# Kernel tuning notes

Measured on AMD Instinct MI355X. Metric: run time of the kernel, lower is better.

Reference implementation:

```python
import jax, jax.numpy as jnp
import numpy as np

B, S, HID = 4, 1024, 4096
NH, NKV, HD = 32, 8, 128
FF = 11008
EPS = 1e-6
THETA = 10000.0


def rms_norm(x, w, eps=EPS):
    v = jnp.mean(jnp.square(x), axis=-1, keepdims=True)
    return x * jax.lax.rsqrt(v + eps) * w


def rotate_half(x):
    x1, x2 = jnp.split(x, 2, axis=-1)
    return jnp.concatenate([-x2, x1], axis=-1)


def rope_cos_sin(position_ids, head_dim=HD, theta=THETA):
    inv_freq = 1.0 / (theta ** (jnp.arange(0, head_dim, 2, dtype=jnp.float32) / head_dim))
    freqs = position_ids.astype(jnp.float32)[..., None] * inv_freq  # [B,S,HD/2]
    emb = jnp.concatenate([freqs, freqs], axis=-1)  # [B,S,HD]
    return jnp.cos(emb)[:, None, :, :], jnp.sin(emb)[:, None, :, :]  # [B,1,S,HD]


def setup_inputs() -> dict:
    key = jax.random.key(0)
    ks = jax.random.split(key, 9)
    sc = 0.02
    pos = jnp.tile(jnp.arange(S, dtype=jnp.int64 if jax.config.jax_enable_x64 else jnp.int32)[None, :], (B, 1))
    causal = jnp.tril(jnp.ones((S, S), dtype=bool))
    mask = jnp.where(causal, 0.0, -1e9).astype(jnp.float32)[None, None]  # [1,1,S,S]
    return {
        "hidden_states": jax.random.normal(ks[0], (B * S, HID), jnp.float32),
        "position_ids": pos,
        "attn_mask": mask,
        "Wq": jax.random.normal(ks[1], (HID, NH * HD), jnp.float32) * sc,
        "Wk": jax.random.normal(ks[2], (HID, NKV * HD), jnp.float32) * sc,
        "Wv": jax.random.normal(ks[3], (HID, NKV * HD), jnp.float32) * sc,
        "Wo": jax.random.normal(ks[4], (NH * HD, HID), jnp.float32) * sc,
        "ln1_w": jnp.ones((HID,), jnp.float32),
        "ln2_w": jnp.ones((HID,), jnp.float32),
        "w_gate": jax.random.normal(ks[5], (HID, FF), jnp.float32) * sc,
        "w_up": jax.random.normal(ks[6], (HID, FF), jnp.float32) * sc,
        "w_down": jax.random.normal(ks[7], (FF, HID), jnp.float32) * sc,
    }


def reference(hidden_states, position_ids, attn_mask, Wq, Wk, Wv, Wo, ln1_w, ln2_w, w_gate, w_up, w_down):
    residual = hidden_states
    h = rms_norm(hidden_states, ln1_w)

    # QKV projections on flat tokens, then reshape per train partition
    q = (h @ Wq).reshape(B, S, NH, HD).transpose(0, 2, 1, 3)     # [B,NH,S,HD]
    k = (h @ Wk).reshape(B, S, NKV, HD).transpose(0, 2, 1, 3)    # [B,NKV,S,HD]
    v = (h @ Wv).reshape(B, S, NKV, HD).transpose(0, 2, 1, 3)

    cos, sin = rope_cos_sin(position_ids)
    q = q * cos + rotate_half(q) * sin
    k = k * cos + rotate_half(k) * sin

    n_rep = NH // NKV
    k = jnp.repeat(k, n_rep, axis=1)  # [B,NH,S,HD]
    v = jnp.repeat(v, n_rep, axis=1)

    scores = jnp.einsum('bhqd,bhkd->bhqk', q, k) / np.sqrt(HD)
    scores = scores + attn_mask
    # softmax in fp32 as in the source
    probs = jax.nn.softmax(scores.astype(jnp.float32), axis=-1).astype(q.dtype)
    attn = jnp.einsum('bhqk,bhkd->bhqd', probs, v)               # [B,NH,S,HD]
    attn = attn.transpose(0, 2, 1, 3).reshape(B * S, NH * HD)
    h = attn @ Wo

    h = residual + h
    residual = h
    h2 = rms_norm(h, ln2_w)
    mlp = (jax.nn.silu(h2 @ w_gate) * (h2 @ w_up)) @ w_down
    return residual + mlp
```

## Files before the change

### kernel.cpp

```cpp
#include <hip/hip_runtime.h>

#define DEVINL __device__ __forceinline__

typedef unsigned short u16;
typedef __attribute__((ext_vector_type(8))) short bf16x8;
typedef __attribute__((ext_vector_type(4))) float f32x4;
typedef __attribute__((ext_vector_type(4))) unsigned short u16x4;


DEVINL float bf2f(u16 u) { union { unsigned i; float f; } x; x.i = ((unsigned)u) << 16; return x.f; }
DEVINL u16 f2bf(float f) {
  union { float f; unsigned i; } x; x.f = f;
  unsigned r = x.i + 0x7fffu + ((x.i >> 16) & 1u);
  return (u16)(r >> 16);
}

DEVINL void async16(u16* lds, const u16* g) {
  __builtin_amdgcn_global_load_lds((const __attribute__((address_space(1))) unsigned*)g,
                                   (__attribute__((address_space(3))) unsigned*)lds, 16, 0, 0);
}

struct CJob { const float* in; u16* out; int K, N, ntiles; int mode; };

DEVINL void conv_one(const float* __restrict__ in, u16* __restrict__ out,
                     int K, int N, int tile, int t, float (*tl)[65], int mode) {
  int tn = N >> 6;
  int kt = tile / tn;
  int k0 = kt << 6, n0 = (tile - kt*tn) << 6;
  int r = t >> 4, c4 = (t & 15) << 2;
  #pragma unroll
  for (int it = 0; it < 4; it++) {
    int row = r + it*16;
    f32x4 v = *(const f32x4*)(in + (size_t)(k0 + row)*N + n0 + c4);
    tl[row][c4+0] = v[0]; tl[row][c4+1] = v[1];
    tl[row][c4+2] = v[2]; tl[row][c4+3] = v[3];
  }
  __syncthreads();
  #pragma unroll
  for (int it = 0; it < 4; it++) {
    int nrow = r + it*16;
    u16x4 ov;
    #pragma unroll
    for (int e = 0; e < 4; e++) ov[e] = f2bf(tl[c4+e][nrow]);
    int orow = n0 + nrow;
    if (mode == 1)      orow = ((orow >> 5) << 6) + (orow & 31);
    else if (mode == 2) orow = ((orow >> 5) << 6) + 32 + (orow & 31);
    *(u16x4*)(out + (size_t)orow*K + k0 + c4) = ov;
  }
  __syncthreads();
}

__global__ __launch_bounds__(256) void conv3(CJob j0, CJob j1, CJob j2) {
  __shared__ float tl[64][65];
  int ntot = j0.ntiles + j1.ntiles + j2.ntiles;
  for (int g = blockIdx.x; g < ntot; g += gridDim.x) {
    CJob* jp;
    int tile;
    if (g < j0.ntiles)                 { jp = &j0; tile = g; }
    else if (g < j0.ntiles + j1.ntiles){ jp = &j1; tile = g - j0.ntiles; }
    else                               { jp = &j2; tile = g - j0.ntiles - j1.ntiles; }
    conv_one(jp->in, jp->out, jp->K, jp->N, tile, threadIdx.x, tl, jp->mode);
  }
}

__global__ __launch_bounds__(256) void conv_t(const float* __restrict__ in,
                                              u16* __restrict__ out, int K, int N) {
  __shared__ float tl[64][65];
  int tile = blockIdx.y * gridDim.x + blockIdx.x;
  conv_one(in, out, K, N, tile, threadIdx.x, tl, 0);
}

__global__ __launch_bounds__(256) void rmsnorm_kernel(const float* __restrict__ x,
                                                      const float* __restrict__ w,
                                                      u16* __restrict__ out) {
  int row = blockIdx.x, t = threadIdx.x;
  const float* xr = x + (size_t)row * 4096;
  f32x4 v[4];
  float ss = 0.f;
  #pragma unroll
  for (int i = 0; i < 4; i++) {
    v[i] = *(const f32x4*)(xr + (t + 256*i)*4);
    ss += v[i][0]*v[i][0] + v[i][1]*v[i][1] + v[i][2]*v[i][2] + v[i][3]*v[i][3];
  }
  #pragma unroll
  for (int d = 1; d < 64; d <<= 1) ss += __shfl_xor(ss, d, 64);
  __shared__ float ps[4];
  if ((t & 63) == 0) ps[t >> 6] = ss;
  __syncthreads();
  float scale = rsqrtf((ps[0]+ps[1]+ps[2]+ps[3]) * (1.f/4096.f) + 1e-6f);
  #pragma unroll
  for (int i = 0; i < 4; i++) {
    f32x4 wv = *(const f32x4*)(w + (t + 256*i)*4);
    u16x4 o;
    #pragma unroll
    for (int e = 0; e < 4; e++) o[e] = f2bf(v[i][e] * scale * wv[e]);
    *(u16x4*)(out + (size_t)row*4096 + (t + 256*i)*4) = o;
  }
}

__global__ __launch_bounds__(256) void rope_kernel(u16* __restrict__ q, u16* __restrict__ k, int kstr) {
  int tok = blockIdx.x;
  int s = tok & 1023;
  __shared__ float cs[64], sn[64];
  int t = threadIdx.x;
  if (t < 64) {
    float inv = __expf(-(float)t * 0.14391156934f);
    float ang = (float)s * inv;
    cs[t] = cosf(ang); sn[t] = sinf(ang);
  }
  __syncthreads();
  const float qscale = 0.08838834764831845f;
  size_t qbase = (size_t)tok * 4096;
  #pragma unroll
  for (int it = 0; it < 8; it++) {
    int item = t + it*256; int h = item >> 6, j = item & 63;
    size_t i0 = qbase + h*128 + j;
    float x1 = bf2f(q[i0]), x2 = bf2f(q[i0+64]);
    float c = cs[j], si = sn[j];
    q[i0]    = f2bf((x1*c - x2*si) * qscale);
    q[i0+64] = f2bf((x2*c + x1*si) * qscale);
  }
  size_t kbase = (size_t)tok * kstr;
  #pragma unroll
  for (int it = 0; it < 2; it++) {
    int item = t + it*256; int h = item >> 6, j = item & 63;
    size_t i0 = kbase + h*128 + j;
    float x1 = bf2f(k[i0]), x2 = bf2f(k[i0+64]);
    float c = cs[j], si = sn[j];
    k[i0]    = f2bf(x1*c - x2*si);
    k[i0+64] = f2bf(x2*c + x1*si);
  }
}

__global__ __launch_bounds__(256) void vtrans(const u16* __restrict__ v, u16* __restrict__ vt, int vstr) {
  __shared__ u16 tile[32][33];
  int bh = blockIdx.z; int b = bh >> 3, kvh = bh & 7;
  int d0 = blockIdx.x << 5, s0 = blockIdx.y << 5;
  int tx = threadIdx.x, ty = threadIdx.y;
  for (int r = ty; r < 32; r += 8)
    tile[r][tx] = v[(size_t)(b*1024 + s0 + r)*vstr + kvh*128 + d0 + tx];
  __syncthreads();
  for (int r = ty; r < 32; r += 8)
    vt[(size_t)((b*8 + kvh)*128 + d0 + r)*1024 + s0 + tx] = tile[tx][r];
}

template<int EPI>
__global__ __launch_bounds__(256, 2) void gemm_bt(
    const u16* __restrict__ A, const u16* __restrict__ Bt,
    void* __restrict__ Cv, const float* __restrict__ resid,
    const u16* __restrict__ gate, int M, int N, int K) {
  __shared__ u16 As[128*64];
  __shared__ u16 Bs[128*64];
  int nwg = gridDim.x;
  int bid = (int)blockIdx.x;
  int cpx = nwg >> 3;
  int swz = (bid & 7) * cpx + (bid >> 3);
  int mt = M >> 7;
  int m0 = (swz % mt) << 7;
  int n0 = (swz / mt) << 7;
  int tid = threadIdx.x;
  int lane = tid & 63, wave = tid >> 6;
  int wm = wave >> 1, wn = wave & 1;

  f32x4 acc[4][4];
  f32x4 zero = {0.f, 0.f, 0.f, 0.f};
  #pragma unroll
  for (int i = 0; i < 4; i++)
    #pragma unroll
    for (int j = 0; j < 4; j++) acc[i][j] = zero;

  int arow[4], acolb[4];
  #pragma unroll
  for (int i = 0; i < 4; i++) {
    int c = i*256 + tid;
    arow[i]  = c >> 3;
    acolb[i] = ((c & 7) * 16) ^ ((arow[i] & 7) << 4);
  }

  int nsteps = K >> 6;
  for (int t = 0; t < nsteps; t++) {
    int k0 = t << 6;
    #pragma unroll
    for (int i = 0; i < 4; i++) {
      async16(As + i*2048 + wave*512, A  + (size_t)(m0 + arow[i])*K + k0 + (acolb[i] >> 1));
      async16(Bs + i*2048 + wave*512, Bt + (size_t)(n0 + arow[i])*K + k0 + (acolb[i] >> 1));
    }
    __syncthreads();
    #pragma unroll
    for (int ks = 0; ks < 2; ks++) {
      bf16x8 af[4], bfr[4];
      int c2 = (ks*32 + (lane >> 4)*8) * 2;
      #pragma unroll
      for (int mf = 0; mf < 4; mf++) {
        int r = wm*64 + mf*16 + (lane & 15);
        af[mf] = *(const bf16x8*)(As + r*64 + ((c2 ^ ((r & 7) << 4)) >> 1));
      }
      #pragma unroll
      for (int nf = 0; nf < 4; nf++) {
        int r = wn*64 + nf*16 + (lane & 15);
        bfr[nf] = *(const bf16x8*)(Bs + r*64 + ((c2 ^ ((r & 7) << 4)) >> 1));
      }
      #pragma unroll
      for (int mf = 0; mf < 4; mf++)
        #pragma unroll
        for (int nf = 0; nf < 4; nf++)
          acc[mf][nf] = __builtin_amdgcn_mfma_f32_16x16x32_bf16(af[mf], bfr[nf], acc[mf][nf], 0, 0, 0);
    }
    __syncthreads();
  }

  #pragma unroll
  for (int mf = 0; mf < 4; mf++)
    #pragma unroll
    for (int nf = 0; nf < 4; nf++)
      #pragma unroll
      for (int j = 0; j < 4; j++) {
        int rr = m0 + wm*64 + mf*16 + (lane >> 4)*4 + j;
        int cc = n0 + wn*64 + nf*16 + (lane & 15);
        size_t idx = (size_t)rr * N + cc;
        float v = acc[mf][nf][j];
        if constexpr (EPI == 0) {
          ((u16*)Cv)[idx] = f2bf(v);
        } else if constexpr (EPI == 1) {
          ((float*)Cv)[idx] = v + resid[idx];
        } else {
          float g = bf2f(gate[idx]);
          float sg = g / (1.f + __expf(-g));
          ((u16*)Cv)[idx] = f2bf(sg * v);
        }
      }
}

#define SB0() __builtin_amdgcn_sched_barrier(0)
#define BAR() __builtin_amdgcn_s_barrier()
#define LGKM(n) do { SB0(); asm volatile("s_waitcnt lgkmcnt(" #n ")" ::: "memory"); SB0(); } while (0)
#define VMC(n)  do { SB0(); asm volatile("s_waitcnt vmcnt(" #n ")"  ::: "memory"); SB0(); } while (0)
#define MFMAQ(qm, qn, AF, BQ) do { \
  __builtin_amdgcn_s_setprio(1); \
  _Pragma("unroll") for (int mf_ = 0; mf_ < 4; mf_++) \
  _Pragma("unroll") for (int nf_ = 0; nf_ < 2; nf_++) \
  _Pragma("unroll") for (int ks_ = 0; ks_ < 2; ks_++) \
    acc[(qm)*4+mf_][(qn)*2+nf_] = __builtin_amdgcn_mfma_f32_16x16x32_bf16( \
        AF[mf_][ks_], BQ[nf_][ks_], acc[(qm)*4+mf_][(qn)*2+nf_], 0, 0, 0); \
  __builtin_amdgcn_s_setprio(0); } while (0)

template<int KC, int EPI>
__global__ __launch_bounds__(512, 2) void gemm256(
    const u16* __restrict__ A, const u16* __restrict__ Bt,
    void* __restrict__ Cv, const float* __restrict__ resid,
    const u16* __restrict__ gate, int M, int N, int G,
    const float* __restrict__ cvin, u16* __restrict__ cvout, int cvK, int cvN, int cvTiles, int cvMode) {
  extern __shared__ u16 lds[];
  int bid = (int)blockIdx.x;
  int tid = threadIdx.x;

  if (bid >= G) {
    int cb = bid - G, CB = (int)gridDim.x - G;
    int h = tid >> 8, t = tid & 255;
    float (*tl)[65] = (float(*)[65])((char*)lds + h*16896);
    int pairs = cvTiles >> 1;
    for (int p = cb; p < pairs; p += CB)
      conv_one(cvin, cvout, cvK, cvN, 2*p + h, t, tl, cvMode);
    return;
  }

  int cpx = G >> 3;
  int swz = (bid & 7) * cpx + (bid >> 3);
  int mt = M >> 8;
  int m0 = (swz % mt) << 8;
  int n0 = (swz / mt) << 8;
  int lane = tid & 63, wave = tid >> 6;
  int wm = wave >> 2, wn = wave & 3;

  f32x4 acc[8][4];
  f32x4 zero = {0.f, 0.f, 0.f, 0.f};
  #pragma unroll
  for (int i = 0; i < 8; i++)
    #pragma unroll
    for (int j = 0; j < 4; j++) acc[i][j] = zero;

  int sCol = ((lane & 7) ^ (lane >> 3)) << 3;
  int aRow = (wave >> 2)*128 + (wave & 3)*16 + (lane >> 3);
  int bRow = (wave >> 1)*64  + (wave & 1)*16 + (lane >> 3);
  const u16* gA = A  + (size_t)(m0 + aRow) * KC + sCol;
  const u16* gB = Bt + (size_t)(n0 + bRow) * KC + sCol;
  constexpr size_t K8 = (size_t)8 * KC, K32 = (size_t)32 * KC, K64 = (size_t)64 * KC;

  int rA = lane & 15;
  int acol0 = (((lane >> 4)    ) ^ (rA & 7)) << 3;
  int acol1 = (((lane >> 4) + 4) ^ (rA & 7)) << 3;

  bf16x8 afA[4][2], afB[4][2], b0[2][2], b1[2][2];

  auto stageAq = [&](int buf, int qm, int k0) {
    u16* d = lds + buf*32768 + qm*8192 + wave*1024;
    const u16* s = gA + (size_t)qm*K64 + k0;
    async16(d, s); async16(d + 512, s + K8);
  };
  auto stageBq = [&](int buf, int qn, int k0) {
    u16* d = lds + buf*32768 + 16384 + qn*8192 + wave*1024;
    const u16* s = gB + (size_t)qn*K32 + k0;
    async16(d, s); async16(d + 512, s + K8);
  };
  auto loadAq = [&](int buf, int qm, bf16x8 (&af)[4][2]) {
    const u16* base = lds + buf*32768 + qm*8192 + wm*4096 + rA*64;
    #pragma unroll
    for (int mf = 0; mf < 4; mf++) {
      af[mf][0] = *(const bf16x8*)(base + mf*1024 + acol0);
      af[mf][1] = *(const bf16x8*)(base + mf*1024 + acol1);
    }
  };
  auto loadBq = [&](int buf, int qn, bf16x8 (&bq)[2][2]) {
    const u16* base = lds + buf*32768 + 16384 + qn*8192 + wn*2048 + rA*64;
    #pragma unroll
    for (int nf = 0; nf < 2; nf++) {
      bq[nf][0] = *(const bf16x8*)(base + nf*1024 + acol0);
      bq[nf][1] = *(const bf16x8*)(base + nf*1024 + acol1);
    }
  };

  constexpr int nt = KC >> 6;
  constexpr int IT = nt/2 - 1;

  stageAq(0, 0, 0); stageBq(0, 0, 0); stageBq(0, 1, 0); stageAq(0, 1, 0);
  VMC(4);
  stageAq(1, 0, 64); stageBq(1, 0, 64); stageBq(1, 1, 64);
  VMC(6);
  BAR();

  #pragma unroll 1
  for (int it = 0; it < IT; it++) {
    int kc = it*128;
    loadAq(0, 0, afA); loadBq(0, 0, b0); stageAq(1, 1, kc + 64);
    LGKM(8); BAR(); LGKM(0);
    MFMAQ(0, 0, afA, b0);
    SB0(); BAR();
    loadBq(0, 1, b1); stageAq(0, 0, kc + 128);
    BAR(); LGKM(0);
    MFMAQ(0, 1, afA, b1);
    SB0(); BAR();
    loadAq(0, 1, afB); stageBq(0, 0, kc + 128);
    BAR(); LGKM(0);
    MFMAQ(1, 0, afB, b0);
    SB0(); BAR();
    stageBq(0, 1, kc + 128);
    BAR();
    MFMAQ(1, 1, afB, b1);
    VMC(6); BAR();
    loadAq(1, 0, afA); loadBq(1, 0, b0); stageAq(0, 1, kc + 128);
    LGKM(8); BAR(); LGKM(0);
    MFMAQ(0, 0, afA, b0);
    SB0(); BAR();
    loadBq(1, 1, b1); stageAq(1, 0, kc + 192);
    BAR(); LGKM(0);
    MFMAQ(0, 1, afA, b1);
    SB0(); BAR();
    loadAq(1, 1, afB); stageBq(1, 0, kc + 192);
    BAR(); LGKM(0);
    MFMAQ(1, 0, afB, b0);
    SB0(); BAR();
    stageBq(1, 1, kc + 192);
    BAR();
    MFMAQ(1, 1, afB, b1);
    VMC(6); BAR();
  }

  {
    int kc = IT*128;
    loadAq(0, 0, afA); loadBq(0, 0, b0); stageAq(1, 1, kc + 64);
    LGKM(8); BAR(); LGKM(0);
    MFMAQ(0, 0, afA, b0);
    SB0(); BAR();
    loadBq(0, 1, b1);
    BAR(); LGKM(0);
    MFMAQ(0, 1, afA, b1);
    SB0(); BAR();
    loadAq(0, 1, afB);
    BAR(); LGKM(0);
    MFMAQ(1, 0, afB, b0);
    SB0(); BAR();
    MFMAQ(1, 1, afB, b1);
    VMC(0); BAR();
    loadAq(1, 0, afA); loadBq(1, 0, b0); SB0();
    loadBq(1, 1, b1); SB0();
    loadAq(1, 1, afB); SB0();
    LGKM(12); MFMAQ(0, 0, afA, b0);
    LGKM(8);  MFMAQ(0, 1, afA, b1);
    LGKM(0);  MFMAQ(1, 0, afB, b0);
    MFMAQ(1, 1, afB, b1);
  }

  if constexpr (EPI == 3) {
    int colb = (n0 >> 1) + wn*32 + (lane & 15);
    #pragma unroll
    for (int mf = 0; mf < 8; mf++)
      #pragma unroll
      for (int nf = 0; nf < 2; nf++)
        #pragma unroll
        for (int j = 0; j < 4; j++) {
          int rr = m0 + wm*128 + mf*16 + (lane >> 4)*4 + j;
          float g = acc[mf][nf][j];
          float u = acc[mf][nf+2][j];
          float sg = g / (1.f + __expf(-g));
          ((u16*)Cv)[(size_t)rr * 11008 + colb + nf*16] = f2bf(sg * u);
        }
  } else {
    #pragma unroll
    for (int mf = 0; mf < 8; mf++)
      #pragma unroll
      for (int nf = 0; nf < 4; nf++)
        #pragma unroll
        for (int j = 0; j < 4; j++) {
          int rr = m0 + wm*128 + mf*16 + (lane >> 4)*4 + j;
          int cc = n0 + wn*64 + nf*16 + (lane & 15);
          size_t idx = (size_t)rr * N + cc;
          float v = acc[mf][nf][j];
          if constexpr (EPI == 0) {
            ((u16*)Cv)[idx] = f2bf(v);
          } else if constexpr (EPI == 1) {
            ((float*)Cv)[idx] = v + resid[idx];
          } else if constexpr (EPI == 2) {
            float g = bf2f(gate[idx]);
            float sg = g / (1.f + __expf(-g));
            ((u16*)Cv)[idx] = f2bf(sg * v);
          }
        }
  }
}

__global__ __launch_bounds__(256, 4) void attn_kernel(
    const u16* __restrict__ q, const u16* __restrict__ k,
    const u16* __restrict__ vt, u16* __restrict__ out,
    CJob j0, CJob j1, CJob j2, int kstr) {
  __shared__ __align__(16) u16 shm[20480];
  u16* Ks = shm;
  u16* Vs = shm + 8192;
  u16* Ps = shm + 16384;
  int bid = blockIdx.x;

  if (bid >= 2048) {
    int cb = bid - 2048, CB = (int)gridDim.x - 2048;
    float (*tl)[65] = (float(*)[65])shm;
    int ntot = j0.ntiles + j1.ntiles + j2.ntiles;
    for (int g = cb; g < ntot; g += CB) {
      CJob* jp; int tile;
      if (g < j0.ntiles)                  { jp = &j0; tile = g; }
      else if (g < j0.ntiles + j1.ntiles) { jp = &j1; tile = g - j0.ntiles; }
      else                                { jp = &j2; tile = g - j0.ntiles - j1.ntiles; }
      conv_one(jp->in, jp->out, jp->K, jp->N, tile, threadIdx.x, tl, jp->mode);
    }
    return;
  }

  int qt = bid & 15;
  int h  = (bid >> 4) & 31;
  int b  = bid >> 9;
  int kvh = h >> 2;
  int tid = threadIdx.x, lane = tid & 63, wave = tid >> 6;
  int q0 = qt << 6;

  bf16x8 qf[4];
  {
    const u16* qb_ = q + (size_t)(b*1024 + q0 + wave*16 + (lane & 15))*4096 + h*128 + (lane >> 4)*8;
    #pragma unroll
    for (int ks = 0; ks < 4; ks++) qf[ks] = *(const bf16x8*)(qb_ + ks*32);
  }
  f32x4 o[8];
  f32x4 zero = {0.f,0.f,0.f,0.f};
  #pragma unroll
  for (int i = 0; i < 8; i++) o[i] = zero;
  float m[4] = {-1e30f,-1e30f,-1e30f,-1e30f};
  float l[4] = {0.f,0.f,0.f,0.f};

  int kr[4], kc[4], vr[4], vc[4];
  #pragma unroll
  for (int i = 0; i < 4; i++) {
    int c = i*256 + tid;
    kr[i] = c >> 4; kc[i] = ((c & 15)*16) ^ ((kr[i] & 7) << 4);
    vr[i] = c >> 3; vc[i] = ((c & 7)*16)  ^ ((vr[i] & 7) << 4);
  }

  for (int t = 0; t <= qt; t++) {
    int kv0 = t << 6;
    #pragma unroll
    for (int i = 0; i < 4; i++) {
      async16(Ks + i*2048 + wave*512, k  + (size_t)(b*1024 + kv0 + kr[i])*kstr + kvh*128 + (kc[i] >> 1));
      async16(Vs + i*2048 + wave*512, vt + (size_t)((b*8 + kvh)*128 + vr[i])*1024 + kv0 + (vc[i] >> 1));
    }
    __syncthreads();

    f32x4 s[4];
    #pragma unroll
    for (int nf = 0; nf < 4; nf++) {
      s[nf] = zero;
      #pragma unroll
      for (int ks = 0; ks < 4; ks++) {
        int r = nf*16 + (lane & 15);
        int c2 = (ks*32 + (lane >> 4)*8)*2;
        bf16x8 kf = *(const bf16x8*)(Ks + r*128 + ((c2 ^ ((r & 7) << 4)) >> 1));
        s[nf] = __builtin_amdgcn_mfma_f32_16x16x32_bf16(qf[ks], kf, s[nf], 0, 0, 0);
      }
    }
    if (t == qt) {
      #pragma unroll
      for (int nf = 0; nf < 4; nf++)
        #pragma unroll
        for (int j = 0; j < 4; j++) {
          int cc = nf*16 + (lane & 15);
          int rr = wave*16 + (lane >> 4)*4 + j;
          if (cc > rr) s[nf][j] = -1e30f;
        }
    }
    #pragma unroll
    for (int j = 0; j < 4; j++) {
      float mx = fmaxf(fmaxf(s[0][j], s[1][j]), fmaxf(s[2][j], s[3][j]));
      #pragma unroll
      for (int d = 1; d < 16; d <<= 1) mx = fmaxf(mx, __shfl_xor(mx, d, 64));
      float mn = fmaxf(m[j], mx);
      float f = __expf(m[j] - mn);
      m[j] = mn;
      float ssum = 0.f;
      #pragma unroll
      for (int nf = 0; nf < 4; nf++) {
        float p = __expf(s[nf][j] - mn);
        s[nf][j] = p; ssum += p;
      }
      #pragma unroll
      for (int d = 1; d < 16; d <<= 1) ssum += __shfl_xor(ssum, d, 64);
      l[j] = l[j]*f + ssum;
      #pragma unroll
      for (int nf = 0; nf < 8; nf++) o[nf][j] *= f;
    }
    #pragma unroll
    for (int nf = 0; nf < 4; nf++)
      #pragma unroll
      for (int j = 0; j < 4; j++) {
        int rr = (lane >> 4)*4 + j;
        int cb2 = ((nf*16 + (lane & 15))*2) ^ ((rr & 7) << 4);
        Ps[wave*1024 + rr*64 + (cb2 >> 1)] = f2bf(s[nf][j]);
      }
    #pragma unroll
    for (int ks2 = 0; ks2 < 2; ks2++) {
      int mr = lane & 15;
      int c2 = (ks2*32 + (lane >> 4)*8)*2;
      bf16x8 pa = *(const bf16x8*)(Ps + wave*1024 + mr*64 + ((c2 ^ ((mr & 7) << 4)) >> 1));
      #pragma unroll
      for (int nf = 0; nf < 8; nf++) {
        int d = nf*16 + (lane & 15);
        bf16x8 vf = *(const bf16x8*)(Vs + d*64 + ((c2 ^ ((d & 7) << 4)) >> 1));
        o[nf] = __builtin_amdgcn_mfma_f32_16x16x32_bf16(pa, vf, o[nf], 0, 0, 0);
      }
    }
    __syncthreads();
  }

  float inv[4];
  #pragma unroll
  for (int j = 0; j < 4; j++) inv[j] = 1.f / l[j];
  u16* ob = out + (size_t)(b*1024 + q0 + wave*16)*4096 + h*128;
  #pragma unroll
  for (int nf = 0; nf < 8; nf++)
    #pragma unroll
    for (int j = 0; j < 4; j++) {
      int rr = (lane >> 4)*4 + j;
      int cc = nf*16 + (lane & 15);
      ob[(size_t)rr*4096 + cc] = f2bf(o[nf][j] * inv[j]);
    }
}

extern "C" void kernel_launch(void* const* d_in, const int* in_sizes, int n_in,
                              void* d_out, int out_size, void* d_ws, size_t ws_size,
                              hipStream_t stream) {
  (void)in_sizes; (void)n_in; (void)out_size;
  const float* hidden = (const float*)d_in[0];
  const float* Wq  = (const float*)d_in[3];
  const float* Wk  = (const float*)d_in[4];
  const float* Wv  = (const float*)d_in[5];
  const float* Wo  = (const float*)d_in[6];
  const float* ln1 = (const float*)d_in[7];
  const float* ln2 = (const float*)d_in[8];
  const float* Wg  = (const float*)d_in[9];
  const float* Wu  = (const float*)d_in[10];
  const float* Wd  = (const float*)d_in[11];
  float* out = (float*)d_out;

  hipFuncSetAttribute((const void*)gemm256<4096,0>,  hipFuncAttributeMaxDynamicSharedMemorySize, 131072);
  hipFuncSetAttribute((const void*)gemm256<4096,1>,  hipFuncAttributeMaxDynamicSharedMemorySize, 131072);
  hipFuncSetAttribute((const void*)gemm256<4096,2>,  hipFuncAttributeMaxDynamicSharedMemorySize, 131072);
  hipFuncSetAttribute((const void*)gemm256<4096,3>,  hipFuncAttributeMaxDynamicSharedMemorySize, 131072);
  hipFuncSetAttribute((const void*)gemm256<11008,1>, hipFuncAttributeMaxDynamicSharedMemorySize, 131072);

  char* ws = (char*)d_ws;
  size_t off = 0;
  auto alloc = [&](size_t b) { char* p = ws + off; off += (b + 4095) & ~(size_t)4095; return p; };

  u16*  wqkvT = (u16*)alloc(50331648);
  u16*  woT   = (u16*)alloc(33554432);
  (void)alloc(8388608);
  u16*  wguT  = (u16*)alloc(180355072);
  u16*  h1    = (u16*)alloc(33554432);
  u16*  qb    = (u16*)alloc(33554432);
  u16*  kvb   = (u16*)alloc(16777216);
  u16*  vtb   = (u16*)alloc(8388608);
  float* hmid = (float*)alloc(67108864);
  u16*  gb    = (u16*)alloc(90177536);
  bool fused = off <= ws_size;

  dim3 blk(256);
  if (fused) {
    u16* wqT  = wqkvT;
    u16* wkvT = wqkvT + 16777216;
    u16* wkT  = wkvT;
    u16* wvT  = wkvT + 4194304;
    u16* wdT  = wqkvT;
    CJob Jq{Wq, wqT, 4096, 4096, 4096, 0}, Jk{Wk, wkT, 4096, 1024, 1024, 0}, Jv{Wv, wvT, 4096, 1024, 1024, 0};
    CJob Jo{Wo, woT, 4096, 4096, 4096, 0};
    CJob Jg{Wg, wguT, 4096, 11008, 11008, 1}, Ju{Wu, wguT, 4096, 11008, 11008, 2};

    conv3<<<2048, blk, 0, stream>>>(Jq, Jk, Jv);
    rmsnorm_kernel<<<4096, blk, 0, stream>>>(hidden, ln1, h1);
    gemm256<4096,0><<<256, 512, 131072, stream>>>(h1, wqT, qb, nullptr, nullptr, 4096, 4096, 256,
                                                  nullptr, nullptr, 0, 0, 0, 0);
    gemm_bt<0><<<512, blk, 0, stream>>>(h1, wkvT, kvb, nullptr, nullptr, 4096, 2048, 4096);
    rope_kernel<<<4096, blk, 0, stream>>>(qb, kvb, 2048);
    vtrans<<<dim3(4, 32, 32), dim3(32, 8), 0, stream>>>(kvb + 1024, vtb, 2048);
    attn_kernel<<<2048 + 1024, blk, 0, stream>>>(qb, kvb, vtb, h1, Jo, Jg, Ju, 2048);
    gemm256<4096,1><<<256, 512, 131072, stream>>>(h1, woT, hmid, hidden, nullptr, 4096, 4096, 256,
                                                  nullptr, nullptr, 0, 0, 0, 0);
    rmsnorm_kernel<<<4096, blk, 0, stream>>>(hmid, ln2, qb);
    gemm256<4096,3><<<1376 + 344, 512, 131072, stream>>>(qb, wguT, gb, nullptr, nullptr, 4096, 11008, 1376,
                                                         Wd, wdT, 11008, 4096, 11008, 0);
    gemm256<11008,1><<<256, 512, 131072, stream>>>(gb, wdT, out, hmid, nullptr, 4096, 4096, 256,
                                                   nullptr, nullptr, 0, 0, 0, 0);
  } else {
    off = 0;
    u16*  W1   = (u16*)alloc(90177536);
    u16*  h1s  = (u16*)alloc(33554432);
    u16*  qbs  = (u16*)alloc(33554432);
    u16*  kvbs = (u16*)alloc(16777216);
    u16*  vtbs = (u16*)alloc(8388608);
    float* hmids = (float*)alloc(67108864);
    u16*  gbs  = (u16*)alloc(90177536);
    if (off > ws_size) return;
    u16* wqT  = W1;
    u16* wkvT = W1 + 16777216;
    conv_t<<<dim3(64, 64),  blk, 0, stream>>>(Wq, wqT, 4096, 4096);
    conv_t<<<dim3(16, 64),  blk, 0, stream>>>(Wk, wkvT, 4096, 1024);
    conv_t<<<dim3(16, 64),  blk, 0, stream>>>(Wv, wkvT + 4194304, 4096, 1024);
    rmsnorm_kernel<<<4096, blk, 0, stream>>>(hidden, ln1, h1s);
    gemm256<4096,0><<<256, 512, 131072, stream>>>(h1s, wqT, qbs, nullptr, nullptr, 4096, 4096, 256,
                                                  nullptr, nullptr, 0, 0, 0, 0);
    gemm_bt<0><<<512, blk, 0, stream>>>(h1s, wkvT, kvbs, nullptr, nullptr, 4096, 2048, 4096);
    rope_kernel<<<4096, blk, 0, stream>>>(qbs, kvbs, 2048);
    vtrans<<<dim3(4, 32, 32), dim3(32, 8), 0, stream>>>(kvbs + 1024, vtbs, 2048);
    CJob J0{nullptr, nullptr, 0, 64, 0, 0};
    attn_kernel<<<2048, blk, 0, stream>>>(qbs, kvbs, vtbs, h1s, J0, J0, J0, 2048);
    conv_t<<<dim3(64, 64), blk, 0, stream>>>(Wo, W1, 4096, 4096);
    gemm256<4096,1><<<256, 512, 131072, stream>>>(h1s, W1, hmids, hidden, nullptr, 4096, 4096, 256,
                                                  nullptr, nullptr, 0, 0, 0, 0);
    rmsnorm_kernel<<<4096, blk, 0, stream>>>(hmids, ln2, qbs);
    conv_t<<<dim3(172, 64), blk, 0, stream>>>(Wg, W1, 4096, 11008);
    gemm256<4096,0><<<688, 512, 131072, stream>>>(qbs, W1, gbs, nullptr, nullptr, 4096, 11008, 688,
                                                  nullptr, nullptr, 0, 0, 0, 0);
    conv_t<<<dim3(172, 64), blk, 0, stream>>>(Wu, W1, 4096, 11008);
    gemm256<4096,2><<<688, 512, 131072, stream>>>(qbs, W1, gbs, nullptr, gbs, 4096, 11008, 688,
                                                  nullptr, nullptr, 0, 0, 0, 0);
    conv_t<<<dim3(64, 172), blk, 0, stream>>>(Wd, W1, 11008, 4096);
    gemm256<11008,1><<<256, 512, 131072, stream>>>(gbs, W1, out, hmids, nullptr, 4096, 4096, 256,
                                                   nullptr, nullptr, 0, 0, 0, 0);
  }
}
```

Measured before the change: 1.625 ms.

## Replace hand-scheduled gemm256 pipeline with a simple double-buffered loop

The hand-interleaved main loop of gemm256 is replaced with a plain double-buffered loop. That loop mixed quarter-tile async LDS staging, explicit lgkm/vm waitcnts, sched barriers and raw s_barriers. The new loop stages the whole next k-slice, computes the current slice with four MFMA quarters, and separates stages with __syncthreads. The unfused fallback path, the conv_t kernel and the unused SiLU-gate epilogue are also removed. The aim is simpler code that leaves scheduling to the compiler, at the cost of less fine-grained overlap and heavier full barriers that wait on all outstanding memory.

```diff
diff --git a/kernel.cpp b/kernel.cpp
--- a/kernel.cpp
+++ b/kernel.cpp
@@ -61,13 +61,6 @@
     else                               { jp = &j2; tile = g - j0.ntiles - j1.ntiles; }
     conv_one(jp->in, jp->out, jp->K, jp->N, tile, threadIdx.x, tl, jp->mode);
   }
-}
-
-__global__ __launch_bounds__(256) void conv_t(const float* __restrict__ in,
-                                              u16* __restrict__ out, int K, int N) {
-  __shared__ float tl[64][65];
-  int tile = blockIdx.y * gridDim.x + blockIdx.x;
-  conv_one(in, out, K, N, tile, threadIdx.x, tl, 0);
 }
 
 __global__ __launch_bounds__(256) void rmsnorm_kernel(const float* __restrict__ x,
@@ -231,10 +224,6 @@
       }
 }
 
-#define SB0() __builtin_amdgcn_sched_barrier(0)
-#define BAR() __builtin_amdgcn_s_barrier()
-#define LGKM(n) do { SB0(); asm volatile("s_waitcnt lgkmcnt(" #n ")" ::: "memory"); SB0(); } while (0)
-#define VMC(n)  do { SB0(); asm volatile("s_waitcnt vmcnt(" #n ")"  ::: "memory"); SB0(); } while (0)
 #define MFMAQ(qm, qn, AF, BQ) do { \
   __builtin_amdgcn_s_setprio(1); \
   _Pragma("unroll") for (int mf_ = 0; mf_ < 4; mf_++) \
@@ -248,7 +237,7 @@
 __global__ __launch_bounds__(512, 2) void gemm256(
     const u16* __restrict__ A, const u16* __restrict__ Bt,
     void* __restrict__ Cv, const float* __restrict__ resid,
-    const u16* __restrict__ gate, int M, int N, int G,
+    int M, int N, int G,
     const float* __restrict__ cvin, u16* __restrict__ cvout, int cvK, int cvN, int cvTiles, int cvMode) {
   extern __shared__ u16 lds[];
   int bid = (int)blockIdx.x;
@@ -302,6 +291,10 @@
     const u16* s = gB + (size_t)qn*K32 + k0;
     async16(d, s); async16(d + 512, s + K8);
   };
+  auto stageAll = [&](int buf, int k0) {
+    stageAq(buf, 0, k0); stageAq(buf, 1, k0);
+    stageBq(buf, 0, k0); stageBq(buf, 1, k0);
+  };
   auto loadAq = [&](int buf, int qm, bf16x8 (&af)[4][2]) {
     const u16* base = lds + buf*32768 + qm*8192 + wm*4096 + rA*64;
     #pragma unroll
@@ -318,76 +311,26 @@
       bq[nf][1] = *(const bf16x8*)(base + nf*1024 + acol1);
     }
   };
+  auto computeTile = [&](int buf) {
+    loadAq(buf, 0, afA); loadBq(buf, 0, b0); loadBq(buf, 1, b1); loadAq(buf, 1, afB);
+    MFMAQ(0, 0, afA, b0);
+    MFMAQ(0, 1, afA, b1);
+    MFMAQ(1, 0, afB, b0);
+    MFMAQ(1, 1, afB, b1);
+  };
 
   constexpr int nt = KC >> 6;
-  constexpr int IT = nt/2 - 1;
-
-  stageAq(0, 0, 0); stageBq(0, 0, 0); stageBq(0, 1, 0); stageAq(0, 1, 0);
-  VMC(4);
-  stageAq(1, 0, 64); stageBq(1, 0, 64); stageBq(1, 1, 64);
-  VMC(6);
-  BAR();
-
+  stageAll(0, 0);
+  __syncthreads();
   #pragma unroll 1
-  for (int it = 0; it < IT; it++) {
-    int kc = it*128;
-    loadAq(0, 0, afA); loadBq(0, 0, b0); stageAq(1, 1, kc + 64);
-    LGKM(8); BAR(); LGKM(0);
-    MFMAQ(0, 0, afA, b0);
-    SB0(); BAR();
-    loadBq(0, 1, b1); stageAq(0, 0, kc + 128);
-    BAR(); LGKM(0);
-    MFMAQ(0, 1, afA, b1);
-    SB0(); BAR();
-    loadAq(0, 1, afB); stageBq(0, 0, kc + 128);
-    BAR(); LGKM(0);
-    MFMAQ(1, 0, afB, b0);
-    SB0(); BAR();
-    stageBq(0, 1, kc + 128);
-    BAR();
-    MFMAQ(1, 1, afB, b1);
-    VMC(6); BAR();
-    loadAq(1, 0, afA); loadBq(1, 0, b0); stageAq(0, 1, kc + 128);
-    LGKM(8); BAR(); LGKM(0);
-    MFMAQ(0, 0, afA, b0);
-    SB0(); BAR();
-    loadBq(1, 1, b1); stageAq(1, 0, kc + 192);
-    BAR(); LGKM(0);
-    MFMAQ(0, 1, afA, b1);
-    SB0(); BAR();
-    loadAq(1, 1, afB); stageBq(1, 0, kc + 192);
-    BAR(); LGKM(0);
-    MFMAQ(1, 0, afB, b0);
-    SB0(); BAR();
-    stageBq(1, 1, kc + 192);
-    BAR();
-    MFMAQ(1, 1, afB, b1);
-    VMC(6); BAR();
-  }
-
-  {
-    int kc = IT*128;
-    loadAq(0, 0, afA); loadBq(0, 0, b0); stageAq(1, 1, kc + 64);
-    LGKM(8); BAR(); LGKM(0);
-    MFMAQ(0, 0, afA, b0);
-    SB0(); BAR();
-    loadBq(0, 1, b1);
-    BAR(); LGKM(0);
-    MFMAQ(0, 1, afA, b1);
-    SB0(); BAR();
-    loadAq(0, 1, afB);
-    BAR(); LGKM(0);
-    MFMAQ(1, 0, afB, b0);
-    SB0(); BAR();
-    MFMAQ(1, 1, afB, b1);
-    VMC(0); BAR();
-    loadAq(1, 0, afA); loadBq(1, 0, b0); SB0();
-    loadBq(1, 1, b1); SB0();
-    loadAq(1, 1, afB); SB0();
-    LGKM(12); MFMAQ(0, 0, afA, b0);
-    LGKM(8);  MFMAQ(0, 1, afA, b1);
-    LGKM(0);  MFMAQ(1, 0, afB, b0);
-    MFMAQ(1, 1, afB, b1);
+  for (int it = 0; it < nt/2; it++) {
+    int kc = it << 7;
+    stageAll(1, kc + 64);
+    computeTile(0);
+    __syncthreads();
+    if (kc + 128 < KC) stageAll(0, kc + 128);
+    computeTile(1);
+    __syncthreads();
   }
 
   if constexpr (EPI == 3) {
@@ -419,10 +362,6 @@
             ((u16*)Cv)[idx] = f2bf(v);
           } else if constexpr (EPI == 1) {
             ((float*)Cv)[idx] = v + resid[idx];
-          } else if constexpr (EPI == 2) {
-            float g = bf2f(gate[idx]);
-            float sg = g / (1.f + __expf(-g));
-            ((u16*)Cv)[idx] = f2bf(sg * v);
           }
         }
   }
@@ -586,7 +525,6 @@
 
   hipFuncSetAttribute((const void*)gemm256<4096,0>,  hipFuncAttributeMaxDynamicSharedMemorySize, 131072);
   hipFuncSetAttribute((const void*)gemm256<4096,1>,  hipFuncAttributeMaxDynamicSharedMemorySize, 131072);
-  hipFuncSetAttribute((const void*)gemm256<4096,2>,  hipFuncAttributeMaxDynamicSharedMemorySize, 131072);
   hipFuncSetAttribute((const void*)gemm256<4096,3>,  hipFuncAttributeMaxDynamicSharedMemorySize, 131072);
   hipFuncSetAttribute((const void*)gemm256<11008,1>, hipFuncAttributeMaxDynamicSharedMemorySize, 131072);
 
@@ -604,69 +542,31 @@
   u16*  vtb   = (u16*)alloc(8388608);
   float* hmid = (float*)alloc(67108864);
   u16*  gb    = (u16*)alloc(90177536);
-  bool fused = off <= ws_size;
+  if (off > ws_size) return;
+
+  u16* wqT  = wqkvT;
+  u16* wkvT = wqkvT + 16777216;
+  u16* wkT  = wkvT;
+  u16* wvT  = wkvT + 4194304;
+  u16* wdT  = wqkvT;
+  CJob Jq{Wq, wqT, 4096, 4096, 4096, 0}, Jk{Wk, wkT, 4096, 1024, 1024, 0}, Jv{Wv, wvT, 4096, 1024, 1024, 0};
+  CJob Jo{Wo, woT, 4096, 4096, 4096, 0};
+  CJob Jg{Wg, wguT, 4096, 11008, 11008, 1}, Ju{Wu, wguT, 4096, 11008, 11008, 2};
 
   dim3 blk(256);
-  if (fused) {
-    u16* wqT  = wqkvT;
-    u16* wkvT = wqkvT + 16777216;
-    u16* wkT  = wkvT;
-    u16* wvT  = wkvT + 4194304;
-    u16* wdT  = wqkvT;
-    CJob Jq{Wq, wqT, 4096, 4096, 4096, 0}, Jk{Wk, wkT, 4096, 1024, 1024, 0}, Jv{Wv, wvT, 4096, 1024, 1024, 0};
-    CJob Jo{Wo, woT, 4096, 4096, 4096, 0};
-    CJob Jg{Wg, wguT, 4096, 11008, 11008, 1}, Ju{Wu, wguT, 4096, 11008, 11008, 2};
-
-    conv3<<<2048, blk, 0, stream>>>(Jq, Jk, Jv);
-    rmsnorm_kernel<<<4096, blk, 0, stream>>>(hidden, ln1, h1);
-    gemm256<4096,0><<<256, 512, 131072, stream>>>(h1, wqT, qb, nullptr, nullptr, 4096, 4096, 256,
-                                                  nullptr, nullptr, 0, 0, 0, 0);
-    gemm_bt<0><<<512, blk, 0, stream>>>(h1, wkvT, kvb, nullptr, nullptr, 4096, 2048, 4096);
-    rope_kernel<<<4096, blk, 0, stream>>>(qb, kvb, 2048);
-    vtrans<<<dim3(4, 32, 32), dim3(32, 8), 0, stream>>>(kvb + 1024, vtb, 2048);
-    attn_kernel<<<2048 + 1024, blk, 0, stream>>>(qb, kvb, vtb, h1, Jo, Jg, Ju, 2048);
-    gemm256<4096,1><<<256, 512, 131072, stream>>>(h1, woT, hmid, hidden, nullptr, 4096, 4096, 256,
-                                                  nullptr, nullptr, 0, 0, 0, 0);
-    rmsnorm_kernel<<<4096, blk, 0, stream>>>(hmid, ln2, qb);
-    gemm256<4096,3><<<1376 + 344, 512, 131072, stream>>>(qb, wguT, gb, nullptr, nullptr, 4096, 11008, 1376,
-                                                         Wd, wdT, 11008, 4096, 11008, 0);
-    gemm256<11008,1><<<256, 512, 131072, stream>>>(gb, wdT, out, hmid, nullptr, 4096, 4096, 256,
-                                                   nullptr, nullptr, 0, 0, 0, 0);
-  } else {
-    off = 0;
-    u16*  W1   = (u16*)alloc(90177536);
-    u16*  h1s  = (u16*)alloc(33554432);
-    u16*  qbs  = (u16*)alloc(33554432);
-    u16*  kvbs = (u16*)alloc(16777216);
-    u16*  vtbs = (u16*)alloc(8388608);
-    float* hmids = (float*)alloc(67108864);
-    u16*  gbs  = (u16*)alloc(90177536);
-    if (off > ws_size) return;
-    u16* wqT  = W1;
-    u16* wkvT = W1 + 16777216;
-    conv_t<<<dim3(64, 64),  blk, 0, stream>>>(Wq, wqT, 4096, 4096);
-    conv_t<<<dim3(16, 64),  blk, 0, stream>>>(Wk, wkvT, 4096, 1024);
-    conv_t<<<dim3(16, 64),  blk, 0, stream>>>(Wv, wkvT + 4194304, 4096, 1024);
-    rmsnorm_kernel<<<4096, blk, 0, stream>>>(hidden, ln1, h1s);
-    gemm256<4096,0><<<256, 512, 131072, stream>>>(h1s, wqT, qbs, nullptr, nullptr, 4096, 4096, 256,
-                                                  nullptr, nullptr, 0, 0, 0, 0);
-    gemm_bt<0><<<512, blk, 0, stream>>>(h1s, wkvT, kvbs, nullptr, nullptr, 4096, 2048, 4096);
-    rope_kernel<<<4096, blk, 0, stream>>>(qbs, kvbs, 2048);
-    vtrans<<<dim3(4, 32, 32), dim3(32, 8), 0, stream>>>(kvbs + 1024, vtbs, 2048);
-    CJob J0{nullptr, nullptr, 0, 64, 0, 0};
-    attn_kernel<<<2048, blk, 0, stream>>>(qbs, kvbs, vtbs, h1s, J0, J0, J0, 2048);
-    conv_t<<<dim3(64, 64), blk, 0, stream>>>(Wo, W1, 4096, 4096);
-    gemm256<4096,1><<<256, 512, 131072, stream>>>(h1s, W1, hmids, hidden, nullptr, 4096, 4096, 256,
-                                                  nullptr, nullptr, 0, 0, 0, 0);
-    rmsnorm_kernel<<<4096, blk, 0, stream>>>(hmids, ln2, qbs);
-    conv_t<<<dim3(172, 64), blk, 0, stream>>>(Wg, W1, 4096, 11008);
-    gemm256<4096,0><<<688, 512, 131072, stream>>>(qbs, W1, gbs, nullptr, nullptr, 4096, 11008, 688,
-                                                  nullptr, nullptr, 0, 0, 0, 0);
-    conv_t<<<dim3(172, 64), blk, 0, stream>>>(Wu, W1, 4096, 11008);
-    gemm256<4096,2><<<688, 512, 131072, stream>>>(qbs, W1, gbs, nullptr, gbs, 4096, 11008, 688,
-                                                  nullptr, nullptr, 0, 0, 0, 0);
-    conv_t<<<dim3(64, 172), blk, 0, stream>>>(Wd, W1, 11008, 4096);
-    gemm256<11008,1><<<256, 512, 131072, stream>>>(gbs, W1, out, hmids, nullptr, 4096, 4096, 256,
-                                                   nullptr, nullptr, 0, 0, 0, 0);
-  }
-}
+  conv3<<<2048, blk, 0, stream>>>(Jq, Jk, Jv);
+  rmsnorm_kernel<<<4096, blk, 0, stream>>>(hidden, ln1, h1);
+  gemm256<4096,0><<<256, 512, 131072, stream>>>(h1, wqT, qb, nullptr, 4096, 4096, 256,
+                                                nullptr, nullptr, 0, 0, 0, 0);
+  gemm_bt<0><<<512, blk, 0, stream>>>(h1, wkvT, kvb, nullptr, nullptr, 4096, 2048, 4096);
+  rope_kernel<<<4096, blk, 0, stream>>>(qb, kvb, 2048);
+  vtrans<<<dim3(4, 32, 32), dim3(32, 8), 0, stream>>>(kvb + 1024, vtb, 2048);
+  attn_kernel<<<2048 + 1024, blk, 0, stream>>>(qb, kvb, vtb, h1, Jo, Jg, Ju, 2048);
+  gemm256<4096,1><<<256, 512, 131072, stream>>>(h1, woT, hmid, hidden, 4096, 4096, 256,
+                                                nullptr, nullptr, 0, 0, 0, 0);
+  rmsnorm_kernel<<<4096, blk, 0, stream>>>(hmid, ln2, qb);
+  gemm256<4096,3><<<1376 + 344, 512, 131072, stream>>>(qb, wguT, gb, nullptr, 4096, 11008, 1376,
+                                                       Wd, wdT, 11008, 4096, 11008, 0);
+  gemm256<11008,1><<<256, 512, 131072, stream>>>(gb, wdT, out, hmid, 4096, 4096, 256,
+                                                 nullptr, nullptr, 0, 0, 0, 0);
+}
```

After: 1.622 ms, median of 2. About the same (-0.2%).
